# Performance work log

Hardware: AMD Instinct MI355X
Metric: run time of the kernel (lower is better)

The kernel has to match this reference:

```python
import jax, jax.numpy as jnp
import numpy as np

N_LAST = 100000
M_CUR = 50000
E = 1600000
F_IN = 64
H = 64  # hidden width of both MLPs


def setup_inputs() -> dict:
    key = jax.random.key(0)
    ks = jax.random.split(key, 12)
    last_coors = jax.random.normal(ks[0], (N_LAST, 3), dtype=jnp.float32)
    last_features = jax.random.normal(ks[1], (N_LAST, F_IN), dtype=jnp.float32)
    current_coors = jax.random.normal(ks[2], (M_CUR, 3), dtype=jnp.float32)
    cur_idx = jax.random.randint(ks[3], (E,), 0, M_CUR, dtype=jnp.int32)
    last_idx = jax.random.randint(ks[4], (E,), 0, N_LAST, dtype=jnp.int32)
    edge = jnp.stack([cur_idx, last_idx], axis=0)
    d_in = F_IN + 3  # 67: features concat relative coords
    def lin(k, fan_in, fan_out):
        bound = 1.0 / np.sqrt(fan_in)
        kw, kb = jax.random.split(k)
        W = jax.random.uniform(kw, (fan_in, fan_out), jnp.float32, -bound, bound)
        b = jax.random.uniform(kb, (fan_out,), jnp.float32, -bound, bound)
        return W, b
    W1, b1 = lin(ks[5], d_in, H)
    W2, b2 = lin(ks[6], H, H)
    W3, b3 = lin(ks[7], H, H)
    W4, b4 = lin(ks[8], H, H)
    return {"last_coors": last_coors, "last_features": last_features,
            "current_coors": current_coors, "edge": edge,
            "W1": W1, "b1": b1, "W2": W2, "b2": b2,
            "W3": W3, "b3": b3, "W4": W4, "b4": b4}


def reference(last_coors, last_features, current_coors, edge,
              W1, b1, W2, b2, W3, b3, W4, b4):
    cur_idx = edge[0]   # [E] indices into current level
    last_idx = edge[1]  # [E] indices into last level
    m = current_coors.shape[0]
    # gather + relative coords concat -> [E, F_IN+3]
    rel = last_coors[last_idx] - current_coors[cur_idx]
    x = jnp.concatenate([last_features[last_idx], rel], axis=1)
    # in_linear: two Linear+ReLU layers
    x = jax.nn.relu(x @ W1 + b1)
    x = jax.nn.relu(x @ W2 + b2)
    # scatter_max into zero-initialized output (torch uses out=zeros, so
    # empty segments stay 0 and max is taken against 0 baseline)
    agg = jax.ops.segment_max(x, cur_idx, num_segments=m)
    agg = jnp.maximum(agg, 0.0)
    # out_linear: two Linear+ReLU layers
    y = jax.nn.relu(agg @ W3 + b3)
    y = jax.nn.relu(y @ W4 + b4)
    return y
```

## Files before the change

kernel.cpp:

```cpp
#include <hip/hip_runtime.h>
#include <hip/hip_fp16.h>

#define FIN 64
#define HH 64
#define BLK 128
#define CIW 32
#define CIWB 5
#define T1 16384
#define RST 65

typedef _Float16 h2v __attribute__((ext_vector_type(2)));
typedef _Float16 f16x8 __attribute__((ext_vector_type(8)));
typedef float f32x4 __attribute__((ext_vector_type(4)));
union U4F { uint4 u; f16x8 h; };

__device__ __forceinline__ unsigned pack2(float x, float y) {
    __half2 h = __floats2half2_rn(x, y);
    union { __half2 h; unsigned u; } z; z.h = h;
    return z.u;
}
__device__ __forceinline__ float2 unpack2(unsigned u) {
    union { unsigned u; __half2 h; } z; z.u = u;
    return __half22float2(z.h);
}
__device__ __forceinline__ float fdot2f(unsigned a, unsigned b, float c) {
#if __has_builtin(__builtin_amdgcn_fdot2)
    union { unsigned u; h2v h; } za, zb; za.u = a; zb.u = b;
    return __builtin_amdgcn_fdot2(za.h, zb.h, c, false);
#else
    float2 fa = unpack2(a), fb = unpack2(b);
    return fmaf(fa.x, fb.x, fmaf(fa.y, fb.y, c));
#endif
}

__device__ __forceinline__ void dot2_layer(const unsigned* lds, int t,
        const unsigned* __restrict__ wp, const float* __restrict__ bias, float* h) {
    #pragma unroll
    for (int j = 0; j < 64; ++j) h[j] = bias[j];
    #pragma unroll 1
    for (int c = 0; c < 8; ++c) {
        uint4 hp = *reinterpret_cast<const uint4*>(&lds[(size_t)t * 32 + ((c ^ (t & 7)) << 2)]);
        const unsigned* w0 = wp + (4 * c + 0) * 64;
        const unsigned* w1 = wp + (4 * c + 1) * 64;
        const unsigned* w2 = wp + (4 * c + 2) * 64;
        const unsigned* w3 = wp + (4 * c + 3) * 64;
        #pragma unroll
        for (int j = 0; j < 64; ++j) {
            float a = fdot2f(hp.x, w0[j], h[j]);
            a = fdot2f(hp.y, w1[j], a);
            a = fdot2f(hp.z, w2[j], a);
            h[j] = fdot2f(hp.w, w3[j], a);
        }
    }
}

__global__ void zero_init(float* agg, int nagg, int* counts, int ncnt) {
    int i = blockIdx.x * blockDim.x + threadIdx.x;
    int stride = gridDim.x * blockDim.x;
    for (int k = i; k < nagg; k += stride) agg[k] = 0.f;
    for (int k = i; k < ncnt; k += stride) counts[k] = 0;
}

__global__ __launch_bounds__(256) void histpack(
    const int* __restrict__ edge, int* bcnt, int E, int NBUK, int NB1,
    const float* __restrict__ W1, const float* __restrict__ W2,
    const float* __restrict__ W3, const float* __restrict__ W4, unsigned* wp) {
    extern __shared__ int lh[];
    int b = blockIdx.x, t = threadIdx.x;
    if (b < NB1) {
        for (int j = t; j < NBUK; j += 256) lh[j] = 0;
        __syncthreads();
        int lo = b * T1, hi = min(lo + T1, E);
        for (int e = lo + t; e < hi; e += 256) atomicAdd(&lh[edge[e] >> CIWB], 1);
        __syncthreads();
        for (int j = t; j < NBUK; j += 256) {
            int c = lh[j];
            if (c) atomicAdd(&bcnt[j], c);
        }
    } else {
        int i = (b - NB1) * 256 + t;
        if (i >= 4 * 2048) return;
        int m = i >> 11, r = i & 2047;
        if (m == 1) {
            int tile = r >> 8;
            int l    = (r >> 2) & 63;
            int p    = r & 3;
            int ni = tile & 3, ks = tile >> 2;
            int col = ni * 16 + (l & 15);
            int k0  = ks * 32 + ((l >> 4) << 3) + 2 * p;
            wp[i] = pack2(W2[k0 * 64 + col], W2[(k0 + 1) * 64 + col]);
        } else {
            int kk = r >> 6, j = r & 63;
            const float* W = (m == 0) ? W1 : (m == 2) ? W3 : W4;
            wp[i] = pack2(W[(2 * kk) * 64 + j], W[(2 * kk + 1) * 64 + j]);
        }
    }
}

__global__ __launch_bounds__(1024) void scan_buckets(const int* __restrict__ bcnt,
                                                     int* bbase, int* bres,
                                                     int NBUK, int E) {
    const int T = 1024;
    int t = threadIdx.x;
    int C = (NBUK + T - 1) / T;
    int lo = t * C, hi = min(lo + C, NBUK);
    int s = 0;
    for (int i = lo; i < hi; ++i) s += bcnt[i];
    __shared__ int ss[T];
    ss[t] = s;
    __syncthreads();
    for (int off = 1; off < T; off <<= 1) {
        int v = (t >= off) ? ss[t - off] : 0;
        __syncthreads();
        ss[t] += v;
        __syncthreads();
    }
    int run = (t == 0) ? 0 : ss[t - 1];
    for (int i = lo; i < hi; ++i) {
        bbase[i] = run;
        bres[i] = run;
        run += bcnt[i];
    }
    if (t == 0) bbase[NBUK] = E;
}

__global__ __launch_bounds__(512) void scatter_prepass(
    const int* __restrict__ edge, int* bres, unsigned* bin, int E, int NBUK, int NB1,
    const float* __restrict__ last_features, const unsigned* __restrict__ w1p,
    const float* __restrict__ b1, uint4* pre1, int N) {
    extern __shared__ int sh[];
    int b = blockIdx.x, t = threadIdx.x;
    if (b < NB1) {
        int* lh = sh;
        int* lofs = sh + NBUK;
        for (int j = t; j < NBUK; j += 512) lh[j] = 0;
        __syncthreads();
        int lo = b * T1, hi = min(lo + T1, E);
        for (int e = lo + t; e < hi; e += 512) atomicAdd(&lh[edge[e] >> CIWB], 1);
        __syncthreads();
        for (int j = t; j < NBUK; j += 512) {
            int c = lh[j];
            lofs[j] = c ? atomicAdd(&bres[j], c) : 0;
            lh[j] = 0;
        }
        __syncthreads();
        for (int e = lo + t; e < hi; e += 512) {
            int ci = edge[e];
            int bk = ci >> CIWB;
            int p = lofs[bk] + atomicAdd(&lh[bk], 1);
            bin[p] = (unsigned)(ci & (CIW - 1)) | ((unsigned)edge[E + e] << CIWB);
        }
    } else {
        int r = (b - NB1) * 512 + t;
        if (r >= N) return;

        const float4* xr = reinterpret_cast<const float4*>(last_features + (size_t)r * FIN);
        float h[64];
        #pragma unroll
        for (int j = 0; j < 64; ++j) h[j] = b1[j];

        #pragma unroll 1
        for (int c = 0; c < 8; ++c) {
            float4 fa = xr[2 * c], fb = xr[2 * c + 1];
            unsigned hp0 = pack2(fa.x, fa.y);
            unsigned hp1 = pack2(fa.z, fa.w);
            unsigned hp2 = pack2(fb.x, fb.y);
            unsigned hp3 = pack2(fb.z, fb.w);
            const unsigned* w0 = w1p + (4 * c + 0) * 64;
            const unsigned* w1 = w1p + (4 * c + 1) * 64;
            const unsigned* w2 = w1p + (4 * c + 2) * 64;
            const unsigned* w3 = w1p + (4 * c + 3) * 64;
            #pragma unroll
            for (int j = 0; j < 64; ++j) {
                float a = fdot2f(hp0, w0[j], h[j]);
                a = fdot2f(hp1, w1[j], a);
                a = fdot2f(hp2, w2[j], a);
                h[j] = fdot2f(hp3, w3[j], a);
            }
        }

        uint4* out = pre1 + (size_t)r * 8;
        #pragma unroll
        for (int c = 0; c < 8; ++c) {
            uint4 o;
            o.x = pack2(h[8 * c + 0], h[8 * c + 1]);
            o.y = pack2(h[8 * c + 2], h[8 * c + 3]);
            o.z = pack2(h[8 * c + 4], h[8 * c + 5]);
            o.w = pack2(h[8 * c + 6], h[8 * c + 7]);
            out[c] = o;
        }
    }
}

__global__ __launch_bounds__(128, 2) void edge_mfma_fused(
    const float* __restrict__ last_coors,
    const float* __restrict__ current_coors,
    const unsigned* __restrict__ bin,
    const uint4* __restrict__ pre1,
    const float* __restrict__ W1,
    const float* __restrict__ b2,
    const unsigned* __restrict__ w2f,
    const int* __restrict__ bbase,
    float* agg, int M, int NBUK)
{
    __shared__ unsigned AstS[2][64 * 32];
    __shared__ int rmxi[CIW * RST];

    int bkt = blockIdx.x, t = threadIdx.x;
    int w = t >> 6, lane = t & 63;
    int lo = bkt * CIW;
    int start = bbase[bkt], end = bbase[bkt + 1];

    for (int i = t; i < CIW * RST; i += 128) rmxi[i] = 0;
    __syncthreads();

    unsigned* Ast = AstS[w];

    f16x8 bf[2][4];
    #pragma unroll
    for (int ks = 0; ks < 2; ++ks)
        #pragma unroll
        for (int ni = 0; ni < 4; ++ni) {
            U4F u;
            u.u = *reinterpret_cast<const uint4*>(w2f + (size_t)((ks * 4 + ni) * 64 + lane) * 4);
            bf[ks][ni] = u.h;
        }
    float bb[4];
    #pragma unroll
    for (int ni = 0; ni < 4; ++ni) bb[ni] = b2[ni * 16 + (lane & 15)];

    const float* rw = W1 + 64 * 64;

    #pragma unroll 1
    for (int s = start + w * 64; s < end; s += 128) {
        int nE = min(64, end - s);

        uint4 q[8] = {};
        float r0 = 0.f, r1 = 0.f, r2 = 0.f;
        int ci = lo;
        if (lane < nE) {
            unsigned bv = bin[s + lane];
            ci = lo + (int)(bv & (CIW - 1));
            int li = (int)(bv >> CIWB);
            const uint4* pr = pre1 + (size_t)li * 8;
            #pragma unroll
            for (int i = 0; i < 8; ++i) q[i] = pr[i];
            r0 = last_coors[3 * li + 0] - current_coors[3 * ci + 0];
            r1 = last_coors[3 * li + 1] - current_coors[3 * ci + 1];
            r2 = last_coors[3 * li + 2] - current_coors[3 * ci + 2];
        }

        #pragma unroll
        for (int c = 0; c < 8; ++c) {
            unsigned qc[4] = {q[c].x, q[c].y, q[c].z, q[c].w};
            unsigned oc[4];
            #pragma unroll
            for (int p = 0; p < 4; ++p) {
                int j0 = 8 * c + 2 * p;
                float2 v = unpack2(qc[p]);
                v.x = fmaf(r0, rw[j0],     fmaf(r1, rw[64 + j0],     fmaf(r2, rw[128 + j0],     v.x)));
                v.y = fmaf(r0, rw[j0 + 1], fmaf(r1, rw[64 + j0 + 1], fmaf(r2, rw[128 + j0 + 1], v.y)));
                oc[p] = pack2(fmaxf(v.x, 0.f), fmaxf(v.y, 0.f));
            }
            uint4 o; o.x = oc[0]; o.y = oc[1]; o.z = oc[2]; o.w = oc[3];
            *reinterpret_cast<uint4*>(&Ast[(size_t)lane * 32 + ((c ^ (lane & 7)) << 2)]) = o;
        }

        f32x4 acc[4][4];
        #pragma unroll
        for (int ni = 0; ni < 4; ++ni)
            #pragma unroll
            for (int mi = 0; mi < 4; ++mi)
                acc[mi][ni] = (f32x4){bb[ni], bb[ni], bb[ni], bb[ni]};

        #pragma unroll
        for (int ks = 0; ks < 2; ++ks) {
            #pragma unroll
            for (int mi = 0; mi < 4; ++mi) {
                int row = mi * 16 + (lane & 15);
                int ch  = (ks * 4 + (lane >> 4)) ^ (row & 7);
                U4F a;
                a.u = *reinterpret_cast<const uint4*>(&Ast[(size_t)row * 32 + (ch << 2)]);
                #pragma unroll
                for (int ni = 0; ni < 4; ++ni)
                    acc[mi][ni] = __builtin_amdgcn_mfma_f32_16x16x32_f16(
                        a.h, bf[ks][ni], acc[mi][ni], 0, 0, 0);
            }
        }

        #pragma unroll
        for (int mi = 0; mi < 4; ++mi) {
            #pragma unroll
            for (int r = 0; r < 4; ++r) {
                int row = mi * 16 + ((lane >> 4) << 2) + r;
                int cir = __shfl(ci, row);
                if (row < nE) {
                    int* dst = &rmxi[(cir - lo) * RST + (lane & 15)];
                    #pragma unroll
                    for (int ni = 0; ni < 4; ++ni)
                        atomicMax(&dst[ni * 16], __float_as_int(acc[mi][ni][r]));
                }
            }
        }
    }
    __syncthreads();

    for (int i = t; i < CIW * 64; i += 128) {
        int gr = lo + (i >> 6);
        if (gr < M) agg[(size_t)gr * 64 + (i & 63)] = __int_as_float(rmxi[(i >> 6) * RST + (i & 63)]);
    }
}

__global__ __launch_bounds__(64, 4) void out_mlp2(
    float* data,
    const unsigned* __restrict__ w3p, const float* __restrict__ b3,
    const unsigned* __restrict__ w4p, const float* __restrict__ b4, int M)
{
    __shared__ unsigned lds[64 * 32];
    int t = threadIdx.x;
    int r = blockIdx.x * 64 + t;
    if (r >= M) return;

    const float4* xr = reinterpret_cast<const float4*>(data + (size_t)r * HH);
    float4 f[16];
    #pragma unroll
    for (int i = 0; i < 16; ++i) f[i] = xr[i];

    #pragma unroll
    for (int c = 0; c < 8; ++c) {
        uint4 o;
        o.x = pack2(f[2 * c].x, f[2 * c].y);
        o.y = pack2(f[2 * c].z, f[2 * c].w);
        o.z = pack2(f[2 * c + 1].x, f[2 * c + 1].y);
        o.w = pack2(f[2 * c + 1].z, f[2 * c + 1].w);
        *reinterpret_cast<uint4*>(&lds[(size_t)t * 32 + ((c ^ (t & 7)) << 2)]) = o;
    }

    float h[64];
    dot2_layer(lds, t, w3p, b3, h);

    #pragma unroll
    for (int c = 0; c < 8; ++c) {
        uint4 o;
        o.x = pack2(fmaxf(h[8 * c + 0], 0.f), fmaxf(h[8 * c + 1], 0.f));
        o.y = pack2(fmaxf(h[8 * c + 2], 0.f), fmaxf(h[8 * c + 3], 0.f));
        o.z = pack2(fmaxf(h[8 * c + 4], 0.f), fmaxf(h[8 * c + 5], 0.f));
        o.w = pack2(fmaxf(h[8 * c + 6], 0.f), fmaxf(h[8 * c + 7], 0.f));
        *reinterpret_cast<uint4*>(&lds[(size_t)t * 32 + ((c ^ (t & 7)) << 2)]) = o;
    }

    float h2[64];
    dot2_layer(lds, t, w4p, b4, h2);

    float4* yr = reinterpret_cast<float4*>(data + (size_t)r * HH);
    #pragma unroll
    for (int c = 0; c < 16; ++c) {
        float4 o;
        o.x = fmaxf(h2[4 * c + 0], 0.f);
        o.y = fmaxf(h2[4 * c + 1], 0.f);
        o.z = fmaxf(h2[4 * c + 2], 0.f);
        o.w = fmaxf(h2[4 * c + 3], 0.f);
        yr[c] = o;
    }
}

__global__ void hist_kernel(const int* __restrict__ edge, int* counts, int E) {
    int e = blockIdx.x * blockDim.x + threadIdx.x;
    if (e < E) atomicAdd(&counts[edge[e]], 1);
}

__global__ __launch_bounds__(1024) void scan_kernel(const int* __restrict__ counts,
                                                    int* cursor, int M) {
    const int T = 1024;
    int t = threadIdx.x;
    int C = (M + T - 1) / T;
    int lo = t * C, hi = min(lo + C, M);
    int s = 0;
    for (int i = lo; i < hi; ++i) s += counts[i];
    __shared__ int ss[T];
    ss[t] = s;
    __syncthreads();
    for (int off = 1; off < T; off <<= 1) {
        int v = (t >= off) ? ss[t - off] : 0;
        __syncthreads();
        ss[t] += v;
        __syncthreads();
    }
    int run = (t == 0) ? 0 : ss[t - 1];
    for (int i = lo; i < hi; ++i) {
        cursor[i] = run;
        run += counts[i];
    }
}

__global__ void scatter_kernel(const int* __restrict__ edge, int* cursor,
                               int* sorted, int E) {
    int e = blockIdx.x * blockDim.x + threadIdx.x;
    if (e < E) {
        int p = atomicAdd(&cursor[edge[e]], 1);
        sorted[p] = e;
    }
}

__global__ __launch_bounds__(BLK) void edge_mlp_sorted(
    const float* __restrict__ last_coors, const float* __restrict__ last_features,
    const float* __restrict__ current_coors, const int* __restrict__ edge,
    const int* __restrict__ sorted,
    const float* __restrict__ W1, const float* __restrict__ b1,
    const float* __restrict__ W2, const float* __restrict__ b2,
    float* agg, int E)
{
    __shared__ float hs[BLK][HH];
    __shared__ int cis[BLK];
    __shared__ int runStart[BLK + 1];
    __shared__ int wl[BLK / 64];
    int base = blockIdx.x * BLK, t = threadIdx.x;
    int nE = min(BLK, E - base);
    int ci = -1, li = 0;
    if (t < nE) { int es = sorted[base + t]; ci = edge[es]; li = edge[E + es]; }
    cis[t] = ci;
    if (t < nE) {
        float h1[HH];
        #pragma unroll
        for (int j = 0; j < HH; ++j) h1[j] = b1[j];
        const float4* xr = reinterpret_cast<const float4*>(last_features + (size_t)li * FIN);
        #pragma unroll 1
        for (int c = 0; c < FIN / 4; ++c) {
            float4 v = xr[c];
            const float* w = W1 + (size_t)(4 * c) * HH;
            #pragma unroll
            for (int j = 0; j < HH; ++j)
                h1[j] = fmaf(v.x, w[j], fmaf(v.y, w[HH + j],
                        fmaf(v.z, w[2 * HH + j], fmaf(v.w, w[3 * HH + j], h1[j]))));
        }
        {
            float r0 = last_coors[3 * li + 0] - current_coors[3 * ci + 0];
            float r1 = last_coors[3 * li + 1] - current_coors[3 * ci + 1];
            float r2 = last_coors[3 * li + 2] - current_coors[3 * ci + 2];
            const float* w = W1 + (size_t)64 * HH;
            #pragma unroll
            for (int j = 0; j < HH; ++j)
                h1[j] = fmaf(r0, w[j], fmaf(r1, w[HH + j], fmaf(r2, w[2 * HH + j], h1[j])));
        }
        #pragma unroll
        for (int c = 0; c < HH / 4; ++c) {
            float4 v;
            v.x = fmaxf(h1[4 * c + 0], 0.f); v.y = fmaxf(h1[4 * c + 1], 0.f);
            v.z = fmaxf(h1[4 * c + 2], 0.f); v.w = fmaxf(h1[4 * c + 3], 0.f);
            int cc = (c + t) & 15;
            *reinterpret_cast<float4*>(&hs[t][cc * 4]) = v;
        }
        float h2[HH];
        #pragma unroll
        for (int j = 0; j < HH; ++j) h2[j] = b2[j];
        #pragma unroll 1
        for (int c = 0; c < HH / 4; ++c) {
            int cc = (c + t) & 15;
            float4 v = *reinterpret_cast<const float4*>(&hs[t][cc * 4]);
            const float* w = W2 + (size_t)(4 * c) * HH;
            #pragma unroll
            for (int j = 0; j < HH; ++j)
                h2[j] = fmaf(v.x, w[j], fmaf(v.y, w[HH + j],
                        fmaf(v.z, w[2 * HH + j], fmaf(v.w, w[3 * HH + j], h2[j]))));
        }
        #pragma unroll
        for (int c = 0; c < HH / 4; ++c) {
            float4 v;
            v.x = fmaxf(h2[4 * c + 0], 0.f); v.y = fmaxf(h2[4 * c + 1], 0.f);
            v.z = fmaxf(h2[4 * c + 2], 0.f); v.w = fmaxf(h2[4 * c + 3], 0.f);
            int cc = (c + t) & 15;
            *reinterpret_cast<float4*>(&hs[t][cc * 4]) = v;
        }
    }
    __syncthreads();
    bool leader = (t < nE) && (t == 0 || cis[t] != cis[t - 1]);
    unsigned long long bal = __ballot(leader);
    int lane = t & 63, wid = t >> 6;
    if (lane == 63) wl[wid] = __popcll(bal);
    __syncthreads();
    int nruns = wl[0] + wl[1];
    if (leader) {
        int ord = __popcll(bal & ((1ull << lane) - 1)) + (wid ? wl[0] : 0);
        runStart[ord] = t;
    }
    if (t == 0) runStart[nruns] = nE;
    __syncthreads();
    int col = t & 63, half = t >> 6;
    int* aggi = reinterpret_cast<int*>(agg);
    for (int r = half; r < nruns; r += BLK / 64) {
        int s = runStart[r], e2 = runStart[r + 1];
        int c2 = cis[s];
        float m = 0.f;
        for (int k = s; k < e2; ++k) {
            int cc = ((col >> 2) + k) & 15;
            m = fmaxf(m, hs[k][cc * 4 + (col & 3)]);
        }
        int addr = c2 * HH + col;
        if (s == 0 || e2 == nE) {
            if (m > 0.f) atomicMax(&aggi[addr], __float_as_int(m));
        } else {
            agg[addr] = m;
        }
    }
}

__global__ __launch_bounds__(BLK) void out_mlp_f32(
    float* data, const float* __restrict__ W3, const float* __restrict__ b3,
    const float* __restrict__ W4, const float* __restrict__ b4, int M)
{
    __shared__ float hsm[BLK][HH];
    int r = blockIdx.x * BLK + threadIdx.x;
    if (r >= M) return;
    int t = threadIdx.x;
    const float4* xr = reinterpret_cast<const float4*>(data + (size_t)r * HH);
    float h[HH];
    #pragma unroll
    for (int j = 0; j < HH; ++j) h[j] = b3[j];
    #pragma unroll 1
    for (int c = 0; c < HH / 4; ++c) {
        float4 v = xr[c];
        const float* w = W3 + (size_t)(4 * c) * HH;
        #pragma unroll
        for (int j = 0; j < HH; ++j)
            h[j] = fmaf(v.x, w[j], fmaf(v.y, w[HH + j],
                   fmaf(v.z, w[2 * HH + j], fmaf(v.w, w[3 * HH + j], h[j]))));
    }
    #pragma unroll
    for (int c = 0; c < HH / 4; ++c) {
        float4 v;
        v.x = fmaxf(h[4 * c + 0], 0.f); v.y = fmaxf(h[4 * c + 1], 0.f);
        v.z = fmaxf(h[4 * c + 2], 0.f); v.w = fmaxf(h[4 * c + 3], 0.f);
        int cc = (c + t) & 15;
        *reinterpret_cast<float4*>(&hsm[t][cc * 4]) = v;
    }
    float h2[HH];
    #pragma unroll
    for (int j = 0; j < HH; ++j) h2[j] = b4[j];
    #pragma unroll 1
    for (int c = 0; c < HH / 4; ++c) {
        int cc = (c + t) & 15;
        float4 v = *reinterpret_cast<const float4*>(&hsm[t][cc * 4]);
        const float* w = W4 + (size_t)(4 * c) * HH;
        #pragma unroll
        for (int j = 0; j < HH; ++j)
            h2[j] = fmaf(v.x, w[j], fmaf(v.y, w[HH + j],
                    fmaf(v.z, w[2 * HH + j], fmaf(v.w, w[3 * HH + j], h2[j]))));
    }
    float* yr = data + (size_t)r * HH;
    #pragma unroll
    for (int c = 0; c < HH / 4; ++c) {
        float4 v;
        v.x = fmaxf(h2[4 * c + 0], 0.f); v.y = fmaxf(h2[4 * c + 1], 0.f);
        v.z = fmaxf(h2[4 * c + 2], 0.f); v.w = fmaxf(h2[4 * c + 3], 0.f);
        *reinterpret_cast<float4*>(&yr[4 * c]) = v;
    }
}

extern "C" void kernel_launch(void* const* d_in, const int* in_sizes, int n_in,
                              void* d_out, int out_size, void* d_ws, size_t ws_size,
                              hipStream_t stream) {
    const float* last_coors    = (const float*)d_in[0];
    const float* last_features = (const float*)d_in[1];
    const float* current_coors = (const float*)d_in[2];
    const int*   edge          = (const int*)d_in[3];
    const float* W1 = (const float*)d_in[4];  const float* b1 = (const float*)d_in[5];
    const float* W2 = (const float*)d_in[6];  const float* b2 = (const float*)d_in[7];
    const float* W3 = (const float*)d_in[8];  const float* b3 = (const float*)d_in[9];
    const float* W4 = (const float*)d_in[10]; const float* b4 = (const float*)d_in[11];

    int E = in_sizes[3] / 2;
    int M = in_sizes[2] / 3;
    int N = in_sizes[0] / 3;

    float* agg = (float*)d_out;
    int NBUK = (M + CIW - 1) / CIW;
    int NB1  = (E + T1 - 1) / T1;
    int PPB  = (N + 511) / 512;

    unsigned* ws = (unsigned*)d_ws;
    size_t offBbase = (size_t)NBUK;
    size_t offBres  = offBbase + NBUK + 1;
    size_t offWp    = (offBres + NBUK + 3) & ~(size_t)3;
    size_t offBin   = offWp + 4 * 2048;
    size_t offPre   = (offBin + (size_t)E + 3) & ~(size_t)3;
    size_t need     = (offPre + (size_t)N * 32) * 4;

    if (ws_size >= need && NBUK <= 4096) {
        int* bcnt     = (int*)ws;
        int* bbase    = (int*)(ws + offBbase);
        int* bres     = (int*)(ws + offBres);
        unsigned* wp  = ws + offWp;
        unsigned* bin = ws + offBin;
        uint4* pre1   = (uint4*)(ws + offPre);

        size_t smem2 = 2 * (size_t)NBUK * 4;

        hipMemsetAsync(bcnt, 0, (size_t)NBUK * 4, stream);
        histpack<<<NB1 + 32, 256, NBUK * 4, stream>>>(edge, bcnt, E, NBUK, NB1,
                                                      W1, W2, W3, W4, wp);
        scan_buckets<<<1, 1024, 0, stream>>>(bcnt, bbase, bres, NBUK, E);
        scatter_prepass<<<NB1 + PPB, 512, smem2, stream>>>(
            edge, bres, bin, E, NBUK, NB1, last_features, wp, b1, pre1, N);
        edge_mfma_fused<<<NBUK, 128, 0, stream>>>(
            last_coors, current_coors, bin, pre1,
            W1, b2, wp + 2048, bbase, agg, M, NBUK);
        out_mlp2<<<(M + 63) / 64, 64, 0, stream>>>(agg, wp + 4096, b3, wp + 6144, b4, M);
    } else {
        int* counts = (int*)ws;
        int* cursor = counts + (M + 1);
        int* sorted = cursor + (M + 1);
        zero_init<<<2048, 256, 0, stream>>>(agg, M * HH, counts, M + 1);
        hist_kernel<<<(E + 255) / 256, 256, 0, stream>>>(edge, counts, E);
        scan_kernel<<<1, 1024, 0, stream>>>(counts, cursor, M);
        scatter_kernel<<<(E + 255) / 256, 256, 0, stream>>>(edge, cursor, sorted, E);
        edge_mlp_sorted<<<(E + BLK - 1) / BLK, BLK, 0, stream>>>(
            last_coors, last_features, current_coors, edge, sorted,
            W1, b1, W2, b2, agg, E);
        out_mlp_f32<<<(M + BLK - 1) / BLK, BLK, 0, stream>>>(agg, W3, b3, W4, b4, M);
    }
}
```

Before: 199.4 us.

## Split edge buckets across two single-wave blocks with partial max buffers

Each 128-thread bucket block becomes two independent 64-thread blocks. Each block handles every other 64-edge chunk of the bucket and writes its own partial segment-max buffer to workspace. The output MLP kernel then merges the two partials with an elementwise max before running layers three and four. This removes the intra-block syncs and gives the scheduler finer-grained blocks, at the cost of an extra partial-result write and read plus more per-block LDS initialisation.

```diff
diff --git a/kernel.cpp b/kernel.cpp
--- a/kernel.cpp
+++ b/kernel.cpp
@@ -192,7 +192,7 @@
     }
 }
 
-__global__ __launch_bounds__(128, 2) void edge_mfma_fused(
+__global__ __launch_bounds__(64, 2) void edge_mfma_fused(
     const float* __restrict__ last_coors,
     const float* __restrict__ current_coors,
     const unsigned* __restrict__ bin,
@@ -201,20 +201,19 @@
     const float* __restrict__ b2,
     const unsigned* __restrict__ w2f,
     const int* __restrict__ bbase,
-    float* agg, int M, int NBUK)
+    float* pout, size_t pmstride,
+    int S, int M, int NBUK)
 {
-    __shared__ unsigned AstS[2][64 * 32];
+    __shared__ unsigned Ast[64 * 32];
     __shared__ int rmxi[CIW * RST];
 
-    int bkt = blockIdx.x, t = threadIdx.x;
-    int w = t >> 6, lane = t & 63;
+    int b = blockIdx.x, t = threadIdx.x;
+    int half = (b >= NBUK) ? 1 : 0;
+    int bkt = b - half * NBUK;
     int lo = bkt * CIW;
     int start = bbase[bkt], end = bbase[bkt + 1];
 
-    for (int i = t; i < CIW * RST; i += 128) rmxi[i] = 0;
-    __syncthreads();
-
-    unsigned* Ast = AstS[w];
+    for (int i = t; i < CIW * RST; i += 64) rmxi[i] = 0;
 
     f16x8 bf[2][4];
     #pragma unroll
@@ -222,24 +221,24 @@
         #pragma unroll
         for (int ni = 0; ni < 4; ++ni) {
             U4F u;
-            u.u = *reinterpret_cast<const uint4*>(w2f + (size_t)((ks * 4 + ni) * 64 + lane) * 4);
+            u.u = *reinterpret_cast<const uint4*>(w2f + (size_t)((ks * 4 + ni) * 64 + t) * 4);
             bf[ks][ni] = u.h;
         }
     float bb[4];
     #pragma unroll
-    for (int ni = 0; ni < 4; ++ni) bb[ni] = b2[ni * 16 + (lane & 15)];
+    for (int ni = 0; ni < 4; ++ni) bb[ni] = b2[ni * 16 + (t & 15)];
 
     const float* rw = W1 + 64 * 64;
 
     #pragma unroll 1
-    for (int s = start + w * 64; s < end; s += 128) {
+    for (int s = start + half * 64; s < end; s += 64 * S) {
         int nE = min(64, end - s);
 
         uint4 q[8] = {};
         float r0 = 0.f, r1 = 0.f, r2 = 0.f;
         int ci = lo;
-        if (lane < nE) {
-            unsigned bv = bin[s + lane];
+        if (t < nE) {
+            unsigned bv = bin[s + t];
             ci = lo + (int)(bv & (CIW - 1));
             int li = (int)(bv >> CIWB);
             const uint4* pr = pre1 + (size_t)li * 8;
@@ -263,7 +262,7 @@
                 oc[p] = pack2(fmaxf(v.x, 0.f), fmaxf(v.y, 0.f));
             }
             uint4 o; o.x = oc[0]; o.y = oc[1]; o.z = oc[2]; o.w = oc[3];
-            *reinterpret_cast<uint4*>(&Ast[(size_t)lane * 32 + ((c ^ (lane & 7)) << 2)]) = o;
+            *reinterpret_cast<uint4*>(&Ast[(size_t)t * 32 + ((c ^ (t & 7)) << 2)]) = o;
         }
 
         f32x4 acc[4][4];
@@ -277,8 +276,8 @@
         for (int ks = 0; ks < 2; ++ks) {
             #pragma unroll
             for (int mi = 0; mi < 4; ++mi) {
-                int row = mi * 16 + (lane & 15);
-                int ch  = (ks * 4 + (lane >> 4)) ^ (row & 7);
+                int row = mi * 16 + (t & 15);
+                int ch  = (ks * 4 + (t >> 4)) ^ (row & 7);
                 U4F a;
                 a.u = *reinterpret_cast<const uint4*>(&Ast[(size_t)row * 32 + (ch << 2)]);
                 #pragma unroll
@@ -292,10 +291,10 @@
         for (int mi = 0; mi < 4; ++mi) {
             #pragma unroll
             for (int r = 0; r < 4; ++r) {
-                int row = mi * 16 + ((lane >> 4) << 2) + r;
+                int row = mi * 16 + ((t >> 4) << 2) + r;
                 int cir = __shfl(ci, row);
                 if (row < nE) {
-                    int* dst = &rmxi[(cir - lo) * RST + (lane & 15)];
+                    int* dst = &rmxi[(cir - lo) * RST + (t & 15)];
                     #pragma unroll
                     for (int ni = 0; ni < 4; ++ni)
                         atomicMax(&dst[ni * 16], __float_as_int(acc[mi][ni][r]));
@@ -303,16 +302,17 @@
             }
         }
     }
-    __syncthreads();
-
-    for (int i = t; i < CIW * 64; i += 128) {
-        int gr = lo + (i >> 6);
-        if (gr < M) agg[(size_t)gr * 64 + (i & 63)] = __int_as_float(rmxi[(i >> 6) * RST + (i & 63)]);
-    }
-}
-
-__global__ __launch_bounds__(64, 4) void out_mlp2(
-    float* data,
+
+    float* outp = pout + (size_t)half * pmstride;
+    #pragma unroll
+    for (int r = 0; r < CIW; ++r) {
+        int gr = lo + r;
+        if (gr < M) outp[(size_t)gr * 64 + t] = __int_as_float(rmxi[r * RST + t]);
+    }
+}
+
+__global__ __launch_bounds__(64, 4) void out_mlp2m(
+    const float* __restrict__ inA, const float* __restrict__ inB, float* out,
     const unsigned* __restrict__ w3p, const float* __restrict__ b3,
     const unsigned* __restrict__ w4p, const float* __restrict__ b4, int M)
 {
@@ -321,10 +321,15 @@
     int r = blockIdx.x * 64 + t;
     if (r >= M) return;
 
-    const float4* xr = reinterpret_cast<const float4*>(data + (size_t)r * HH);
+    const float4* xa = reinterpret_cast<const float4*>(inA + (size_t)r * HH);
+    const float4* xb = reinterpret_cast<const float4*>(inB + (size_t)r * HH);
     float4 f[16];
     #pragma unroll
-    for (int i = 0; i < 16; ++i) f[i] = xr[i];
+    for (int i = 0; i < 16; ++i) {
+        float4 a = xa[i], b = xb[i];
+        f[i].x = fmaxf(a.x, b.x); f[i].y = fmaxf(a.y, b.y);
+        f[i].z = fmaxf(a.z, b.z); f[i].w = fmaxf(a.w, b.w);
+    }
 
     #pragma unroll
     for (int c = 0; c < 8; ++c) {
@@ -352,7 +357,7 @@
     float h2[64];
     dot2_layer(lds, t, w4p, b4, h2);
 
-    float4* yr = reinterpret_cast<float4*>(data + (size_t)r * HH);
+    float4* yr = reinterpret_cast<float4*>(out + (size_t)r * HH);
     #pragma unroll
     for (int c = 0; c < 16; ++c) {
         float4 o;
@@ -583,15 +588,24 @@
     size_t offWp    = (offBres + NBUK + 3) & ~(size_t)3;
     size_t offBin   = offWp + 4 * 2048;
     size_t offPre   = (offBin + (size_t)E + 3) & ~(size_t)3;
-    size_t need     = (offPre + (size_t)N * 32) * 4;
-
-    if (ws_size >= need && NBUK <= 4096) {
+    size_t offPm    = offPre + (size_t)N * 32;
+    size_t pmstride = (size_t)NBUK * CIW * 64;
+    size_t needS2   = (offPm + 2 * pmstride) * 4;
+    size_t needS1   = offPm * 4;
+
+    if (ws_size >= needS1 && NBUK <= 4096) {
         int* bcnt     = (int*)ws;
         int* bbase    = (int*)(ws + offBbase);
         int* bres     = (int*)(ws + offBres);
         unsigned* wp  = ws + offWp;
         unsigned* bin = ws + offBin;
         uint4* pre1   = (uint4*)(ws + offPre);
+        float* pmax   = (float*)(ws + offPm);
+
+        bool split = (ws_size >= needS2);
+        int S = split ? 2 : 1;
+        float* pout = split ? pmax : agg;
+        size_t pstr = split ? pmstride : 0;
 
         size_t smem2 = 2 * (size_t)NBUK * 4;
 
@@ -601,10 +615,15 @@
         scan_buckets<<<1, 1024, 0, stream>>>(bcnt, bbase, bres, NBUK, E);
         scatter_prepass<<<NB1 + PPB, 512, smem2, stream>>>(
             edge, bres, bin, E, NBUK, NB1, last_features, wp, b1, pre1, N);
-        edge_mfma_fused<<<NBUK, 128, 0, stream>>>(
+        edge_mfma_fused<<<S * NBUK, 64, 0, stream>>>(
             last_coors, current_coors, bin, pre1,
-            W1, b2, wp + 2048, bbase, agg, M, NBUK);
-        out_mlp2<<<(M + 63) / 64, 64, 0, stream>>>(agg, wp + 4096, b3, wp + 6144, b4, M);
+            W1, b2, wp + 2048, bbase, pout, pstr, S, M, NBUK);
+        if (split)
+            out_mlp2m<<<(M + 63) / 64, 64, 0, stream>>>(
+                pmax, pmax + pmstride, agg, wp + 4096, b3, wp + 6144, b4, M);
+        else
+            out_mlp2m<<<(M + 63) / 64, 64, 0, stream>>>(
+                agg, agg, agg, wp + 4096, b3, wp + 6144, b4, M);
     } else {
         int* counts = (int*)ws;
         int* cursor = counts + (M + 1);
```

After: 201.0 us. Within noise of the previous version (+0.8%).

## Use single-wave blocks in edge kernel with software-prefetched gathers

Applied to the files above, without the earlier changes.

The per-bucket edge kernel now runs one 64-thread wavefront per block instead of two, which removes the block-level barriers and halves the shared staging buffer. It software-pipelines the gather: the next tile's pre1 rows and relative coordinates are loaded while the current tile goes through the MFMA and atomic-max steps, and bin indices are read two tiles ahead. The goal is to hide gather latency and sync cost. In exchange it uses more registers, and each block does serial work over its bucket with less intra-block parallelism.

```diff
diff --git a/kernel.cpp b/kernel.cpp
--- a/kernel.cpp
+++ b/kernel.cpp
@@ -8,6 +8,7 @@
 #define CIWB 5
 #define T1 16384
 #define RST 65
+#define INVB 0xFFFFFFFFu
 
 typedef _Float16 h2v __attribute__((ext_vector_type(2)));
 typedef _Float16 f16x8 __attribute__((ext_vector_type(8)));
@@ -192,7 +193,7 @@
     }
 }
 
-__global__ __launch_bounds__(128, 2) void edge_mfma_fused(
+__global__ __launch_bounds__(64, 2) void edge_mfma_fused(
     const float* __restrict__ last_coors,
     const float* __restrict__ current_coors,
     const unsigned* __restrict__ bin,
@@ -203,18 +204,14 @@
     const int* __restrict__ bbase,
     float* agg, int M, int NBUK)
 {
-    __shared__ unsigned AstS[2][64 * 32];
+    __shared__ unsigned Ast[64 * 32];
     __shared__ int rmxi[CIW * RST];
 
     int bkt = blockIdx.x, t = threadIdx.x;
-    int w = t >> 6, lane = t & 63;
     int lo = bkt * CIW;
     int start = bbase[bkt], end = bbase[bkt + 1];
 
-    for (int i = t; i < CIW * RST; i += 128) rmxi[i] = 0;
-    __syncthreads();
-
-    unsigned* Ast = AstS[w];
+    for (int i = t; i < CIW * RST; i += 64) rmxi[i] = 0;
 
     f16x8 bf[2][4];
     #pragma unroll
@@ -222,33 +219,36 @@
         #pragma unroll
         for (int ni = 0; ni < 4; ++ni) {
             U4F u;
-            u.u = *reinterpret_cast<const uint4*>(w2f + (size_t)((ks * 4 + ni) * 64 + lane) * 4);
+            u.u = *reinterpret_cast<const uint4*>(w2f + (size_t)((ks * 4 + ni) * 64 + t) * 4);
             bf[ks][ni] = u.h;
         }
     float bb[4];
     #pragma unroll
-    for (int ni = 0; ni < 4; ++ni) bb[ni] = b2[ni * 16 + (lane & 15)];
+    for (int ni = 0; ni < 4; ++ni) bb[ni] = b2[ni * 16 + (t & 15)];
 
     const float* rw = W1 + 64 * 64;
 
+    unsigned bvA = (start + t < end) ? bin[start + t] : INVB;
+    unsigned bvB = (start + 64 + t < end) ? bin[start + 64 + t] : INVB;
+    uint4 q[8] = {};
+    float rr0 = 0.f, rr1 = 0.f, rr2 = 0.f;
+    if (bvA != INVB) {
+        int li = (int)(bvA >> CIWB);
+        int ci0 = lo + (int)(bvA & (CIW - 1));
+        const uint4* pr = pre1 + (size_t)li * 8;
+        #pragma unroll
+        for (int i = 0; i < 8; ++i) q[i] = pr[i];
+        rr0 = last_coors[3 * li + 0] - current_coors[3 * ci0 + 0];
+        rr1 = last_coors[3 * li + 1] - current_coors[3 * ci0 + 1];
+        rr2 = last_coors[3 * li + 2] - current_coors[3 * ci0 + 2];
+    }
+
     #pragma unroll 1
-    for (int s = start + w * 64; s < end; s += 128) {
+    for (int s = start; s < end; s += 64) {
         int nE = min(64, end - s);
-
-        uint4 q[8] = {};
-        float r0 = 0.f, r1 = 0.f, r2 = 0.f;
-        int ci = lo;
-        if (lane < nE) {
-            unsigned bv = bin[s + lane];
-            ci = lo + (int)(bv & (CIW - 1));
-            int li = (int)(bv >> CIWB);
-            const uint4* pr = pre1 + (size_t)li * 8;
-            #pragma unroll
-            for (int i = 0; i < 8; ++i) q[i] = pr[i];
-            r0 = last_coors[3 * li + 0] - current_coors[3 * ci + 0];
-            r1 = last_coors[3 * li + 1] - current_coors[3 * ci + 1];
-            r2 = last_coors[3 * li + 2] - current_coors[3 * ci + 2];
-        }
+        int ci = (bvA != INVB) ? (lo + (int)(bvA & (CIW - 1))) : lo;
+
+        unsigned bvC = (s + 128 + t < end) ? bin[s + 128 + t] : INVB;
 
         #pragma unroll
         for (int c = 0; c < 8; ++c) {
@@ -258,12 +258,27 @@
             for (int p = 0; p < 4; ++p) {
                 int j0 = 8 * c + 2 * p;
                 float2 v = unpack2(qc[p]);
-                v.x = fmaf(r0, rw[j0],     fmaf(r1, rw[64 + j0],     fmaf(r2, rw[128 + j0],     v.x)));
-                v.y = fmaf(r0, rw[j0 + 1], fmaf(r1, rw[64 + j0 + 1], fmaf(r2, rw[128 + j0 + 1], v.y)));
+                v.x = fmaf(rr0, rw[j0],     fmaf(rr1, rw[64 + j0],     fmaf(rr2, rw[128 + j0],     v.x)));
+                v.y = fmaf(rr0, rw[j0 + 1], fmaf(rr1, rw[64 + j0 + 1], fmaf(rr2, rw[128 + j0 + 1], v.y)));
                 oc[p] = pack2(fmaxf(v.x, 0.f), fmaxf(v.y, 0.f));
             }
             uint4 o; o.x = oc[0]; o.y = oc[1]; o.z = oc[2]; o.w = oc[3];
-            *reinterpret_cast<uint4*>(&Ast[(size_t)lane * 32 + ((c ^ (lane & 7)) << 2)]) = o;
+            *reinterpret_cast<uint4*>(&Ast[(size_t)t * 32 + ((c ^ (t & 7)) << 2)]) = o;
+        }
+
+        if (bvB != INVB) {
+            int lin = (int)(bvB >> CIWB);
+            int cin = lo + (int)(bvB & (CIW - 1));
+            const uint4* prn = pre1 + (size_t)lin * 8;
+            #pragma unroll
+            for (int i = 0; i < 8; ++i) q[i] = prn[i];
+            rr0 = last_coors[3 * lin + 0] - current_coors[3 * cin + 0];
+            rr1 = last_coors[3 * lin + 1] - current_coors[3 * cin + 1];
+            rr2 = last_coors[3 * lin + 2] - current_coors[3 * cin + 2];
+        } else {
+            #pragma unroll
+            for (int i = 0; i < 8; ++i) q[i] = make_uint4(0, 0, 0, 0);
+            rr0 = rr1 = rr2 = 0.f;
         }
 
         f32x4 acc[4][4];
@@ -277,8 +292,8 @@
         for (int ks = 0; ks < 2; ++ks) {
             #pragma unroll
             for (int mi = 0; mi < 4; ++mi) {
-                int row = mi * 16 + (lane & 15);
-                int ch  = (ks * 4 + (lane >> 4)) ^ (row & 7);
+                int row = mi * 16 + (t & 15);
+                int ch  = (ks * 4 + (t >> 4)) ^ (row & 7);
                 U4F a;
                 a.u = *reinterpret_cast<const uint4*>(&Ast[(size_t)row * 32 + (ch << 2)]);
                 #pragma unroll
@@ -292,22 +307,25 @@
         for (int mi = 0; mi < 4; ++mi) {
             #pragma unroll
             for (int r = 0; r < 4; ++r) {
-                int row = mi * 16 + ((lane >> 4) << 2) + r;
+                int row = mi * 16 + ((t >> 4) << 2) + r;
                 int cir = __shfl(ci, row);
                 if (row < nE) {
-                    int* dst = &rmxi[(cir - lo) * RST + (lane & 15)];
+                    int* dst = &rmxi[(cir - lo) * RST + (t & 15)];
                     #pragma unroll
                     for (int ni = 0; ni < 4; ++ni)
                         atomicMax(&dst[ni * 16], __float_as_int(acc[mi][ni][r]));
                 }
             }
         }
-    }
-    __syncthreads();
-
-    for (int i = t; i < CIW * 64; i += 128) {
-        int gr = lo + (i >> 6);
-        if (gr < M) agg[(size_t)gr * 64 + (i & 63)] = __int_as_float(rmxi[(i >> 6) * RST + (i & 63)]);
+
+        bvA = bvB;
+        bvB = bvC;
+    }
+
+    #pragma unroll
+    for (int r = 0; r < CIW; ++r) {
+        int gr = lo + r;
+        if (gr < M) agg[(size_t)gr * 64 + t] = __int_as_float(rmxi[r * RST + t]);
     }
 }
 
@@ -601,7 +619,7 @@
         scan_buckets<<<1, 1024, 0, stream>>>(bcnt, bbase, bres, NBUK, E);
         scatter_prepass<<<NB1 + PPB, 512, smem2, stream>>>(
             edge, bres, bin, E, NBUK, NB1, last_features, wp, b1, pre1, N);
-        edge_mfma_fused<<<NBUK, 128, 0, stream>>>(
+        edge_mfma_fused<<<NBUK, 64, 0, stream>>>(
             last_coors, current_coors, bin, pre1,
             W1, b2, wp + 2048, bbase, agg, M, NBUK);
         out_mlp2<<<(M + 63) / 64, 64, 0, stream>>>(agg, wp + 4096, b3, wp + 6144, b4, M);
```

Result: faster. 188.7 us, median of 2 (-5.4%).
